# Optimization experiments

Measured on AMD Instinct MI355X. Metric: run time of the kernel, lower is better.

## Reference

```python
import jax, jax.numpy as jnp
import numpy as np

B, L = 8, 1024
VOCAB, D_ENC, D_MAIN = 260, 128, 256
N_ENC, N_MAIN, N_DEC, N_HEADS = 3, 6, 3, 4
N_RATIO = 6.0  # 1/target_ratio
NEG = jnp.float32(-1e9)


def setup_inputs() -> dict:
    key = jax.random.key(0)
    kc = iter(jax.random.split(key, 40))
    def nrm(shape, std):
        return jax.random.normal(next(kc), shape, jnp.float32) * std
    inp = {'byte_ids': jax.random.randint(next(kc), (B, L), 0, VOCAB)}
    inp['embed'] = nrm((VOCAB, D_ENC), D_ENC ** -0.5)
    eye = jnp.eye(D_ENC, dtype=jnp.float32)
    inp['wq'] = eye + nrm((D_ENC, D_ENC), 0.02)  # init is identity in the torch module
    inp['wk'] = eye + nrm((D_ENC, D_ENC), 0.02)
    inp['proj_up'] = nrm((D_MAIN, D_ENC), D_ENC ** -0.5)
    inp['proj_down'] = nrm((D_ENC, D_MAIN), 1e-3)
    inp['norm_w'] = jnp.ones((D_ENC,), jnp.float32)
    inp['norm_b'] = jnp.zeros((D_ENC,), jnp.float32)
    for pre, n, d in [('enc', N_ENC, D_ENC), ('main', N_MAIN, D_MAIN), ('dec', N_DEC, D_ENC)]:
        inp[pre + '_ln1_w'] = jnp.ones((n, d), jnp.float32)
        inp[pre + '_ln1_b'] = jnp.zeros((n, d), jnp.float32)
        inp[pre + '_qkv'] = nrm((n, 3 * d, d), d ** -0.5)   # MHA in_proj (3D, D)
        inp[pre + '_wo'] = nrm((n, d, d), d ** -0.5)        # MHA out_proj
        inp[pre + '_ln2_w'] = jnp.ones((n, d), jnp.float32)
        inp[pre + '_ln2_b'] = jnp.zeros((n, d), jnp.float32)
        inp[pre + '_w1'] = nrm((n, 2 * d, d), d ** -0.5)    # mlp_mult = 2
        inp[pre + '_w2'] = nrm((n, d, 2 * d), (2 * d) ** -0.5)
    return inp


def _ln(x, w, b):
    mu = jnp.mean(x, axis=-1, keepdims=True)
    var = jnp.mean((x - mu) ** 2, axis=-1, keepdims=True)
    return (x - mu) * jax.lax.rsqrt(var + 1e-5) * w + b


def _mha(x, wqkv, wo, bias):
    Bb, S, D = x.shape
    dh = D // N_HEADS
    q, k, v = jnp.split(x @ wqkv.T, 3, axis=-1)
    q = q.reshape(Bb, S, N_HEADS, dh)
    k = k.reshape(Bb, S, N_HEADS, dh)
    v = v.reshape(Bb, S, N_HEADS, dh)
    scores = jnp.einsum('bqhd,bkhd->bhqk', q, k) * (dh ** -0.5) + bias
    attn = jax.nn.softmax(scores, axis=-1)
    out = jnp.einsum('bhqk,bkhd->bqhd', attn, v).reshape(Bb, S, D)
    return out @ wo.T


def _block(x, stack, i, bias):
    ln1w, ln1b, qkv, wo, ln2w, ln2b, w1, w2 = (a[i] for a in stack)
    x = x + _mha(_ln(x, ln1w, ln1b), qkv, wo, bias)
    h = _ln(x, ln2w, ln2b)
    return x + jax.nn.gelu(h @ w1.T, approximate=False) @ w2.T


def _downsample(x, b_hard):
    # scatter boundary tokens to the front of a padded (B, S, D) buffer
    Bb, S, D = x.shape
    idx = jnp.cumsum(b_hard, axis=1).astype(jnp.int32) - 1
    dest = jnp.where(b_hard > 0.5, idx, S)  # S is out-of-range -> dropped
    def sc(xb, db):
        return jnp.zeros((S, D), xb.dtype).at[db].set(xb, mode='drop')
    out = jax.vmap(sc)(x, dest)
    counts = jnp.sum(b_hard, axis=1).astype(jnp.int32)
    mask = jnp.arange(S)[None, :] < counts[:, None]
    return out, mask


def _forward(byte_ids, embed, wq, wk,
             enc_ln1_w, enc_ln1_b, enc_qkv, enc_wo, enc_ln2_w, enc_ln2_b, enc_w1, enc_w2,
             proj_up,
             main_ln1_w, main_ln1_b, main_qkv, main_wo, main_ln2_w, main_ln2_b, main_w1, main_w2,
             proj_down,
             dec_ln1_w, dec_ln1_b, dec_qkv, dec_wo, dec_ln2_w, dec_ln2_b, dec_w1, dec_w2,
             norm_w, norm_b):
    causal = jnp.where(jnp.triu(jnp.ones((L, L), bool), 1), NEG, jnp.float32(0.0))[None, None]
    x = embed[byte_ids]  # (B, L, D_ENC)
    enc_p = (enc_ln1_w, enc_ln1_b, enc_qkv, enc_wo, enc_ln2_w, enc_ln2_b, enc_w1, enc_w2)
    for i in range(N_ENC):
        x = _block(x, enc_p, i, causal)

    # --- dynamic chunking (routing + ratio loss) ---
    def l2n(t):
        return t / jnp.maximum(jnp.linalg.norm(t, axis=-1, keepdims=True), 1e-12)
    q = l2n(x @ wq.T)
    k = l2n(x @ wk.T)
    k_prev = jnp.pad(k[:, :-1], ((0, 0), (1, 0), (0, 0)))
    cos = jnp.sum(q * k_prev, axis=-1)
    p = jnp.clip(0.5 * (1.0 - cos), 0.0, 1.0)
    p = jnp.concatenate([jnp.ones_like(p[:, :1]), p[:, 1:]], axis=1)
    b_hard = (p >= 0.5).astype(jnp.float32)
    N = N_RATIO
    F_act = jnp.mean(b_hard)
    G_act = jnp.mean(p)
    ratio_loss = N / (N - 1.0) * ((N - 1.0) * F_act * G_act + (1.0 - F_act) * (1.0 - G_act))
    compressed, comp_mask = _downsample(x, b_hard)
    p_comp = _downsample(p[..., None], b_hard)[0][..., 0]

    # --- main stack on compressed sequence (padded to L, masked) ---
    z = compressed @ proj_up.T
    main_bias = causal + jnp.where(comp_mask, jnp.float32(0.0), NEG)[:, None, None, :]
    main_p = (main_ln1_w, main_ln1_b, main_qkv, main_wo, main_ln2_w, main_ln2_b, main_w1, main_w2)
    for i in range(N_MAIN):
        z = _block(z, main_p, i, main_bias)
    z = z @ proj_down.T  # (B, L, D_ENC)

    # --- chunk-level EMA (parallel linear-recurrence scan) + gather + STE ---
    p_c = jnp.clip(p_comp, 1e-4, 1.0 - 1e-4)
    a = (1.0 - p_c).at[:, 0].set(0.0)[..., None]          # z_bar[0] = z[0]
    bv = (p_c[..., None] * z).at[:, :1].set(z[:, :1])
    def comb(lhs, rhs):
        al, bl = lhs
        ar, br = rhs
        return (al * ar, ar * bl + br)
    z_bar = jax.lax.associative_scan(comb, (a, bv), axis=1)[1]
    chunk_idx = jnp.clip(jnp.cumsum(b_hard, axis=1).astype(jnp.int32) - 1, 0, None)
    z_up = jnp.take_along_axis(z_bar, jnp.broadcast_to(chunk_idx[:, :, None], z_bar.shape), axis=1)
    c = b_hard * p + (1.0 - b_hard) * (1.0 - p)
    c_ste = c + jax.lax.stop_gradient(1.0 - c)
    x = x + c_ste[..., None] * z_up

    dec_p = (dec_ln1_w, dec_ln1_b, dec_qkv, dec_wo, dec_ln2_w, dec_ln2_b, dec_w1, dec_w2)
    for i in range(N_DEC):
        x = _block(x, dec_p, i, causal)
    x = _ln(x, norm_w, norm_b)
    logits = x @ embed.T  # tied head
    return logits, ratio_loss


def reference(byte_ids, embed, wq, wk,
              enc_ln1_w, enc_ln1_b, enc_qkv, enc_wo, enc_ln2_w, enc_ln2_b, enc_w1, enc_w2,
              proj_up,
              main_ln1_w, main_ln1_b, main_qkv, main_wo, main_ln2_w, main_ln2_b, main_w1, main_w2,
              proj_down,
              dec_ln1_w, dec_ln1_b, dec_qkv, dec_wo, dec_ln2_w, dec_ln2_b, dec_w1, dec_w2,
              norm_w, norm_b):
    return _forward(byte_ids, embed, wq, wk,
                    enc_ln1_w, enc_ln1_b, enc_qkv, enc_wo, enc_ln2_w, enc_ln2_b, enc_w1, enc_w2,
                    proj_up,
                    main_ln1_w, main_ln1_b, main_qkv, main_wo, main_ln2_w, main_ln2_b, main_w1, main_w2,
                    proj_down,
                    dec_ln1_w, dec_ln1_b, dec_qkv, dec_wo, dec_ln2_w, dec_ln2_b, dec_w1, dec_w2,
                    norm_w, norm_b)
```

## Files before the change

kernel.cpp:

```cpp
#include <hip/hip_runtime.h>
#include <hip/hip_bf16.h>

#define B_ 8
#define L_ 1024
#define BL (B_*L_)
#define DENC 128
#define DMAIN 256
#define VOCAB 260
#define NHEADS 4

typedef __hip_bfloat16 bf16;
typedef _Float16 f16;
typedef f16 half8 __attribute__((ext_vector_type(8)));
typedef f16 half4 __attribute__((ext_vector_type(4)));
typedef f16 half2v __attribute__((ext_vector_type(2)));
typedef float f32x4 __attribute__((ext_vector_type(4)));

__global__ __launch_bounds__(64) void k_detect(const void* __restrict__ emb, int* __restrict__ flag){
    int lane = threadIdx.x;
    const unsigned short* u = (const unsigned short*)emb;
    int bad = 0;
    #pragma unroll
    for (int j = 0; j < 4; j++){
        unsigned short h = u[lane + 64*j];
        bf16 t = *(const bf16*)&h;
        float v = __bfloat162float(t);
        if (!(fabsf(v) < 1e4f)) bad++;
    }
    #pragma unroll
    for (int o = 32; o >= 1; o >>= 1) bad += __shfl_xor(bad, o);
    if (lane == 0) flag[0] = (bad == 0) ? 1 : 0;
}

struct CvtArgs {
    const void* src[31];
    unsigned offs[32];
};
__global__ void k_cvt_all(CvtArgs a, float* __restrict__ dst, f16* __restrict__ dst16,
                          int total, const int* __restrict__ flag, unsigned f32mask){
    int isbf = flag[0];
    for (int i = blockIdx.x*256 + threadIdx.x; i < total; i += gridDim.x*256){
        int lo = 0, hi = 30;
        while (lo < hi){ int mid = (lo+hi+1)>>1; if (a.offs[mid] <= (unsigned)i) lo = mid; else hi = mid-1; }
        int j = i - (int)a.offs[lo];
        float v = isbf ? __bfloat162float(((const bf16*)a.src[lo])[j])
                       : ((const float*)a.src[lo])[j];
        if ((f32mask >> lo) & 1u) dst[i] = v;
        dst16[i] = (f16)v;
    }
}

__global__ __launch_bounds__(256) void k_embed_ln(const int* __restrict__ ids, const float* __restrict__ emb,
        const float* __restrict__ lnw, const float* __restrict__ lnb,
        float* __restrict__ x, f16* __restrict__ y){
    int row = blockIdx.x*4 + (threadIdx.x >> 6);
    int lane = threadIdx.x & 63;
    int id = ids[row];
    float v0 = emb[(size_t)id*DENC + lane];
    float v1 = emb[(size_t)id*DENC + 64 + lane];
    x[(size_t)row*DENC + lane] = v0;
    x[(size_t)row*DENC + 64 + lane] = v1;
    float s = v0 + v1;
    #pragma unroll
    for (int o=32;o>=1;o>>=1) s += __shfl_xor(s,o);
    float mu = s / (float)DENC;
    float d0 = v0-mu, d1 = v1-mu;
    float s2 = d0*d0 + d1*d1;
    #pragma unroll
    for (int o=32;o>=1;o>>=1) s2 += __shfl_xor(s2,o);
    float inv = rsqrtf(s2/(float)DENC + 1e-5f);
    y[(size_t)row*DENC + lane]      = (f16)(d0*inv*lnw[lane] + lnb[lane]);
    y[(size_t)row*DENC + 64 + lane] = (f16)(d1*inv*lnw[64+lane] + lnb[64+lane]);
}

template<int D>
__global__ __launch_bounds__(256) void k_ln16(const float* __restrict__ x, const float* __restrict__ w,
                                              const float* __restrict__ b, f16* __restrict__ y){
    int row = blockIdx.x*4 + (threadIdx.x >> 6);
    int lane = threadIdx.x & 63;
    const float* xr = x + (size_t)row*D;
    float v[D/64];
    float s = 0.f;
    #pragma unroll
    for (int j=0;j<D/64;j++){ v[j] = xr[lane + j*64]; s += v[j]; }
    #pragma unroll
    for (int o=32;o>=1;o>>=1) s += __shfl_xor(s,o);
    float mu = s / (float)D;
    float s2 = 0.f;
    #pragma unroll
    for (int j=0;j<D/64;j++){ float dd = v[j]-mu; s2 += dd*dd; }
    #pragma unroll
    for (int o=32;o>=1;o>>=1) s2 += __shfl_xor(s2,o);
    float inv = rsqrtf(s2/(float)D + 1e-5f);
    f16* yr = y + (size_t)row*D;
    #pragma unroll
    for (int j=0;j<D/64;j++){
        int d = lane + j*64;
        yr[d] = (f16)((v[j]-mu)*inv*w[d] + b[d]);
    }
}

#define GBM 64
#define GBN 64
#define GBK 32
__global__ __launch_bounds__(256) void k_gemm2(const float* __restrict__ A, const float* __restrict__ Wq,
        const float* __restrict__ Wk, float* __restrict__ Cq, float* __restrict__ Ck, int K)
{
    __shared__ float As[GBK][GBM+4];
    __shared__ float Ws[GBK][GBN+4];
    int tid = threadIdx.x;
    int bm = blockIdx.y * GBM;
    int bn = blockIdx.x * GBN;
    int tx = tid & 15, ty = tid >> 4;
    float acc[4][4] = {};
    for (int k0 = 0; k0 < K; k0 += GBK){
        #pragma unroll
        for (int i = tid; i < GBM*GBK; i += 256){
            int m = i >> 5, kk = i & 31;
            As[kk][m] = A[(size_t)(bm+m)*K + k0 + kk];
        }
        #pragma unroll
        for (int i = tid; i < GBN*GBK; i += 256){
            int n = i >> 5, kk = i & 31;
            int gn = bn + n;
            const float* W = (gn < 128) ? Wq : Wk;
            int wr = gn & 127;
            Ws[kk][n] = W[(size_t)wr*K + k0 + kk];
        }
        __syncthreads();
        #pragma unroll
        for (int kk = 0; kk < GBK; kk++){
            float a0[4], w0[4];
            *(float4*)a0 = *(const float4*)&As[kk][ty*4];
            *(float4*)w0 = *(const float4*)&Ws[kk][tx*4];
            #pragma unroll
            for (int i=0;i<4;i++)
                #pragma unroll
                for (int j=0;j<4;j++) acc[i][j] += a0[i]*w0[j];
        }
        __syncthreads();
    }
    #pragma unroll
    for (int i=0;i<4;i++){
        int m = bm + ty*4 + i;
        #pragma unroll
        for (int j=0;j<4;j++){
            int n = bn + tx*4 + j;
            float* C = (n < 128) ? Cq : Ck;
            C[(size_t)m*128 + (n & 127)] = acc[i][j];
        }
    }
}

template<int K>
__global__ __launch_bounds__(256) void k_hgemm(const f16* __restrict__ A, const f16* __restrict__ W,
        const float* __restrict__ R, float* __restrict__ C, f16* __restrict__ C16,
        void* __restrict__ OutRaw, const int* __restrict__ flag, int N, int mode,
        f16* __restrict__ Qd, f16* __restrict__ Kd, f16* __restrict__ Vd,
        int dShift, int dhShift)
{
    __shared__ half8 As[4][64];
    __shared__ half8 Ws[4][64];
    int tid = threadIdx.x;
    int wave = tid >> 6, lane = tid & 63;
    int wr = wave >> 1, wc = wave & 1;
    int quad = lane >> 4, l15 = lane & 15;
    int bm = blockIdx.y * 64, bn = blockIdx.x * 64;

    f32x4 acc[2][2] = {};
    int srow = tid >> 2, sc8 = tid & 3;
    const f16* ap0 = A + (size_t)(bm + srow)*K + sc8*8;
    int gn = bn + srow;
    const f16* wp0 = W + (size_t)gn*K + sc8*8;
    bool wok = (gn < N);

    for (int k0 = 0; k0 < K; k0 += 32){
        __syncthreads();
        As[sc8][srow] = *(const half8*)(ap0 + k0);
        Ws[sc8][srow] = wok ? *(const half8*)(wp0 + k0) : (half8)(f16)0.f;
        __syncthreads();
        half8 af[2], wf[2];
        af[0] = As[quad][wr*32 + l15];
        af[1] = As[quad][wr*32 + 16 + l15];
        wf[0] = Ws[quad][wc*32 + l15];
        wf[1] = Ws[quad][wc*32 + 16 + l15];
        #pragma unroll
        for (int i=0;i<2;i++)
            #pragma unroll
            for (int j=0;j<2;j++)
                acc[i][j] = __builtin_amdgcn_mfma_f32_16x16x32_f16(af[i], wf[j], acc[i][j], 0, 0, 0);
    }

    #pragma unroll
    for (int j=0;j<2;j++){
        int n = bn + wc*32 + j*16 + l15;
        if (n >= N) continue;
        #pragma unroll
        for (int i=0;i<2;i++){
            #pragma unroll
            for (int r=0;r<4;r++){
                int m = bm + wr*32 + i*16 + quad*4 + r;
                float v = acc[i][j][r];
                if (mode == 5){
                    int which = n >> dShift;
                    int rem = n & ((1<<dShift)-1);
                    int hh = rem >> dhShift;
                    int dd = rem & ((1<<dhShift)-1);
                    int bb = m >> 10, tt = m & 1023;
                    int Hn = 1 << (dShift - dhShift);
                    f16* dst = (which==0) ? Qd : ((which==1) ? Kd : Vd);
                    if (which == 2)
                        dst[((((size_t)bb*Hn + hh) << dhShift) + dd)*L_ + tt] = (f16)v;
                    else
                        dst[((((size_t)bb*Hn + hh)*L_ + tt) << dhShift) + dd] = (f16)v;
                    continue;
                }
                size_t off = (size_t)m*N + n;
                if (mode == 1){ C[off] = v + R[off]; }
                else if (mode == 2){
                    v = 0.5f*v*(1.0f + erff(v*0.70710678118654752f));
                    C16[off] = (f16)v;
                } else if (mode == 3){
                    if (flag[0]) ((bf16*)OutRaw)[off] = __float2bfloat16(v);
                    else         ((float*)OutRaw)[off] = v;
                } else C[off] = v;
            }
        }
    }
}

template<int K, int N>
__global__ __launch_bounds__(256) void k_gfl(const f16* __restrict__ A, const f16* __restrict__ W,
        const float* __restrict__ R, float* __restrict__ X, f16* __restrict__ Y,
        const float* __restrict__ lnw, const float* __restrict__ lnb, int doLN, int hasR)
{
    constexpr int NT2 = N/32;
    __shared__ half8 As[4][32];
    __shared__ half8 Ws[4][N];
    __shared__ float sred[2][2][32];
    int tid = threadIdx.x;
    int wave = tid >> 6, lane = tid & 63;
    int wr = wave >> 1, wc = wave & 1;
    int quad = lane >> 4, l15 = lane & 15;
    int bm = blockIdx.x * 32;

    f32x4 acc[NT2] = {};
    int srow = (tid & 127) >> 2, sch = tid & 3;
    const f16* ap0 = A + (size_t)(bm + srow)*K + sch*8;
    int s4 = tid >> 2;

    for (int k0 = 0; k0 < K; k0 += 32){
        __syncthreads();
        if (tid < 128) As[sch][srow] = *(const half8*)(ap0 + k0);
        #pragma unroll
        for (int s = 0; s < N/64; s++){
            int rr = s4 + s*64;
            Ws[sch][rr] = *(const half8*)(W + (size_t)rr*K + sch*8 + k0);
        }
        __syncthreads();
        half8 af = As[quad][wr*16 + l15];
        #pragma unroll
        for (int j=0;j<NT2;j++){
            half8 wf = Ws[quad][(wc*NT2 + j)*16 + l15];
            acc[j] = __builtin_amdgcn_mfma_f32_16x16x32_f16(af, wf, acc[j], 0, 0, 0);
        }
    }

    float v[NT2][4];
    #pragma unroll
    for (int r=0;r<4;r++){
        int row = bm + wr*16 + quad*4 + r;
        #pragma unroll
        for (int j=0;j<NT2;j++){
            int col = (wc*NT2 + j)*16 + l15;
            float rv = hasR ? R[(size_t)row*N + col] : 0.f;
            v[j][r] = acc[j][r] + rv;
            X[(size_t)row*N + col] = v[j][r];
        }
    }
    if (doLN){
        int lrow0 = wr*16 + quad*4;
        float mu[4], inv[4];
        #pragma unroll
        for (int r=0;r<4;r++){
            float s = 0.f;
            #pragma unroll
            for (int j=0;j<NT2;j++) s += v[j][r];
            s += __shfl_xor(s, 1); s += __shfl_xor(s, 2);
            s += __shfl_xor(s, 4); s += __shfl_xor(s, 8);
            if (l15 == 0) sred[0][wc][lrow0 + r] = s;
        }
        __syncthreads();
        #pragma unroll
        for (int r=0;r<4;r++)
            mu[r] = (sred[0][0][lrow0 + r] + sred[0][1][lrow0 + r]) / (float)N;
        #pragma unroll
        for (int r=0;r<4;r++){
            float s2 = 0.f;
            #pragma unroll
            for (int j=0;j<NT2;j++){ float dd = v[j][r] - mu[r]; s2 += dd*dd; }
            s2 += __shfl_xor(s2, 1); s2 += __shfl_xor(s2, 2);
            s2 += __shfl_xor(s2, 4); s2 += __shfl_xor(s2, 8);
            if (l15 == 0) sred[1][wc][lrow0 + r] = s2;
        }
        __syncthreads();
        #pragma unroll
        for (int r=0;r<4;r++)
            inv[r] = rsqrtf((sred[1][0][lrow0 + r] + sred[1][1][lrow0 + r]) / (float)N + 1e-5f);
        float wv_[NT2], bv_[NT2];
        #pragma unroll
        for (int j=0;j<NT2;j++){
            int col = (wc*NT2 + j)*16 + l15;
            wv_[j] = lnw[col];
            bv_[j] = lnb[col];
        }
        #pragma unroll
        for (int r=0;r<4;r++){
            int row = bm + wr*16 + quad*4 + r;
            #pragma unroll
            for (int j=0;j<NT2;j++){
                int col = (wc*NT2 + j)*16 + l15;
                Y[(size_t)row*N + col] = (f16)((v[j][r] - mu[r])*inv[r]*wv_[j] + bv_[j]);
            }
        }
    }
}

template<int K>
__global__ __launch_bounds__(256) void k_lngemm(const float* __restrict__ A, const f16* __restrict__ W,
        const float* __restrict__ lnw, const float* __restrict__ lnb, int doLN,
        float* __restrict__ C, void* __restrict__ OutRaw,
        const int* __restrict__ flag, int N, int mode)
{
    constexpr int SA = K + 8;
    constexpr int RPT = K/64;
    __shared__ f16 sA[64*SA];
    int tid = threadIdx.x;
    int wave = tid >> 6, lane = tid & 63;
    int wr = wave >> 1, wc = wave & 1;
    int quad = lane >> 4, l15 = lane & 15;
    int bm = blockIdx.y * 64, bn = blockIdx.x * 64;

    float wv_[RPT], bv_[RPT];
    #pragma unroll
    for (int j=0;j<RPT;j++){
        int d = lane*RPT + j;
        wv_[j] = doLN ? lnw[d] : 1.f;
        bv_[j] = doLN ? lnb[d] : 0.f;
    }
    for (int rr=0; rr<16; rr++){
        int row = wave*16 + rr;
        const float* xr = A + (size_t)(bm+row)*K + lane*RPT;
        float v[RPT];
        if (RPT==2){ float2 t = *(const float2*)xr; v[0]=t.x; v[1]=t.y; }
        else       { float4 t = *(const float4*)xr; v[0]=t.x; v[1]=t.y; v[2]=t.z; v[3]=t.w; }
        float mu = 0.f, inv = 1.f;
        if (doLN){
            float s=0.f;
            #pragma unroll
            for (int j=0;j<RPT;j++) s += v[j];
            #pragma unroll
            for (int o=32;o>=1;o>>=1) s += __shfl_xor(s,o);
            mu = s / (float)K;
            float s2=0.f;
            #pragma unroll
            for (int j=0;j<RPT;j++){ float dd=v[j]-mu; s2+=dd*dd; }
            #pragma unroll
            for (int o=32;o>=1;o>>=1) s2 += __shfl_xor(s2,o);
            inv = rsqrtf(s2/(float)K + 1e-5f);
        }
        if (RPT==2){
            half2v h;
            h[0]=(f16)((v[0]-mu)*inv*wv_[0]+bv_[0]);
            h[1]=(f16)((v[1]-mu)*inv*wv_[1]+bv_[1]);
            *(half2v*)&sA[row*SA + lane*2] = h;
        } else {
            half4 h;
            #pragma unroll
            for (int j=0;j<4;j++) h[j]=(f16)((v[j]-mu)*inv*wv_[j]+bv_[j]);
            *(half4*)&sA[row*SA + lane*4] = h;
        }
    }
    __syncthreads();

    f32x4 acc[2][2] = {};
    int n0 = bn + wc*32 + l15;
    bool ok0 = n0 < N, ok1 = (n0+16) < N;
    const f16* w0p = W + (size_t)n0*K + quad*8;
    const f16* w1p = W + (size_t)(n0+16)*K + quad*8;
    #pragma unroll 4
    for (int k0=0;k0<K;k0+=32){
        half8 af[2], wf[2];
        af[0] = *(const half8*)&sA[(wr*32 + l15)*SA + k0 + quad*8];
        af[1] = *(const half8*)&sA[(wr*32 + 16 + l15)*SA + k0 + quad*8];
        wf[0] = ok0 ? *(const half8*)(w0p + k0) : (half8)(f16)0.f;
        wf[1] = ok1 ? *(const half8*)(w1p + k0) : (half8)(f16)0.f;
        #pragma unroll
        for (int i=0;i<2;i++)
            #pragma unroll
            for (int j=0;j<2;j++)
                acc[i][j] = __builtin_amdgcn_mfma_f32_16x16x32_f16(af[i], wf[j], acc[i][j], 0, 0, 0);
    }

    #pragma unroll
    for (int j=0;j<2;j++){
        int n = bn + wc*32 + j*16 + l15;
        if (n >= N) continue;
        #pragma unroll
        for (int i=0;i<2;i++){
            #pragma unroll
            for (int r=0;r<4;r++){
                int m = bm + wr*32 + i*16 + quad*4 + r;
                float v = acc[i][j][r];
                size_t off = (size_t)m*N + n;
                if (mode == 3){
                    if (flag[0]) ((bf16*)OutRaw)[off] = __float2bfloat16(v);
                    else         ((float*)OutRaw)[off] = v;
                } else C[off] = v;
            }
        }
    }
}

template<int DH>
__global__ __launch_bounds__(256) void k_mflash(const f16* __restrict__ Qh, const f16* __restrict__ Kh,
        const f16* __restrict__ Vt, f16* __restrict__ out, const int* __restrict__ counts,
        float scale)
{
    constexpr int BQ = 64, BK = 64;
    constexpr int RS = DH + 8;
    constexpr int PS = BK + 8;
    __shared__ f16 sQ[BQ*RS];
    __shared__ f16 sK[BK*RS];
    __shared__ f16 sVt[DH*PS];
    __shared__ f16 sP[BQ*PS];

    int x = blockIdx.x, b = x >> 2, h = x & 3;
    int yy = blockIdx.y;
    int qt = (yy < 8) ? yy : 23 - yy;
    int q0 = qt * BQ;
    int tid = threadIdx.x;
    int wv = tid >> 6, lane = tid & 63;
    int quad = lane >> 4, l15 = lane & 15;

    const f16* Qb = Qh + (size_t)x*L_*DH;
    const f16* Kb = Kh + (size_t)x*L_*DH;
    const f16* Vb = Vt + (size_t)x*DH*L_;
    int kcap = counts ? counts[b] : L_;
    int klen = min(kcap, q0 + BQ);

    for (int i = tid; i < BQ*DH/8; i += 256){
        int r = (8*i)/DH, c = (8*i)%DH;
        *(half8*)&sQ[r*RS + c] = *(const half8*)&Qb[(size_t)(q0+r)*DH + c];
    }

    float m[4], l[4];
    #pragma unroll
    for (int r=0;r<4;r++){ m[r] = -1e30f; l[r] = 0.f; }
    f32x4 accO[DH/16] = {};

    for (int k0 = 0; k0 < klen; k0 += BK){
        __syncthreads();
        for (int i = tid; i < BK*DH/8; i += 256){
            int r = (8*i)/DH, c = (8*i)%DH;
            *(half8*)&sK[r*RS + c] = *(const half8*)&Kb[(size_t)(k0+r)*DH + c];
        }
        for (int i = tid; i < DH*BK/8; i += 256){
            int r = (8*i)/BK, c = (8*i)%BK;
            *(half8*)&sVt[r*PS + c] = *(const half8*)&Vb[(size_t)r*L_ + k0 + c];
        }
        __syncthreads();

        half8 af[DH/32];
        #pragma unroll
        for (int ds=0; ds<DH/32; ds++)
            af[ds] = *(const half8*)&sQ[(16*wv + l15)*RS + quad*8 + 32*ds];
        f32x4 accS[4] = {};
        #pragma unroll
        for (int t=0;t<4;t++){
            #pragma unroll
            for (int ds=0; ds<DH/32; ds++){
                half8 bf = *(const half8*)&sK[(16*t + l15)*RS + quad*8 + 32*ds];
                accS[t] = __builtin_amdgcn_mfma_f32_16x16x32_f16(af[ds], bf, accS[t], 0, 0, 0);
            }
        }

        #pragma unroll
        for (int r=0;r<4;r++){
            int qrow = q0 + 16*wv + quad*4 + r;
            float sv[4];
            #pragma unroll
            for (int t=0;t<4;t++){
                float v = accS[t][r]*scale;
                int kp = k0 + 16*t + l15;
                if (kp > qrow || kp >= kcap) v = -1e30f;
                sv[t] = v;
            }
            float rm = fmaxf(fmaxf(sv[0],sv[1]), fmaxf(sv[2],sv[3]));
            rm = fmaxf(rm, __shfl_xor(rm, 1));
            rm = fmaxf(rm, __shfl_xor(rm, 2));
            rm = fmaxf(rm, __shfl_xor(rm, 4));
            rm = fmaxf(rm, __shfl_xor(rm, 8));
            float mn = fmaxf(m[r], rm);
            float al = __expf(m[r] - mn);
            float p0 = __expf(sv[0]-mn), p1 = __expf(sv[1]-mn);
            float p2 = __expf(sv[2]-mn), p3 = __expf(sv[3]-mn);
            float rs = p0+p1+p2+p3;
            rs += __shfl_xor(rs, 1);
            rs += __shfl_xor(rs, 2);
            rs += __shfl_xor(rs, 4);
            rs += __shfl_xor(rs, 8);
            l[r] = l[r]*al + rs;
            m[r] = mn;
            #pragma unroll
            for (int dt=0; dt<DH/16; dt++) accO[dt][r] *= al;
            int prow = 16*wv + quad*4 + r;
            sP[prow*PS + 16*0 + l15] = (f16)p0;
            sP[prow*PS + 16*1 + l15] = (f16)p1;
            sP[prow*PS + 16*2 + l15] = (f16)p2;
            sP[prow*PS + 16*3 + l15] = (f16)p3;
        }

        half8 pf[2];
        #pragma unroll
        for (int ks=0; ks<2; ks++)
            pf[ks] = *(const half8*)&sP[(16*wv + l15)*PS + quad*8 + 32*ks];
        #pragma unroll
        for (int dt=0; dt<DH/16; dt++){
            #pragma unroll
            for (int ks=0; ks<2; ks++){
                half8 bv = *(const half8*)&sVt[(16*dt + l15)*PS + quad*8 + 32*ks];
                accO[dt] = __builtin_amdgcn_mfma_f32_16x16x32_f16(pf[ks], bv, accO[dt], 0, 0, 0);
            }
        }
    }

    #pragma unroll
    for (int r=0;r<4;r++){
        float inv = 1.0f / l[r];
        int qrow = q0 + 16*wv + quad*4 + r;
        #pragma unroll
        for (int dt=0; dt<DH/16; dt++){
            int d = 16*dt + l15;
            out[((size_t)b*L_ + qrow)*(NHEADS*DH) + h*DH + d] = (f16)(accO[dt][r]*inv);
        }
    }
}

__global__ __launch_bounds__(64) void k_router(const float* __restrict__ Q, const float* __restrict__ Kr,
        float* __restrict__ p, float* __restrict__ bh, float* __restrict__ acc)
{
    int idx = blockIdx.x;
    int t = idx & (L_-1);
    int lane = threadIdx.x;
    if (idx == 0 && lane < 8) acc[lane] = 0.f;
    float pv;
    if (t == 0){ pv = 1.0f; }
    else {
        const float* qr = Q  + (size_t)idx*DENC;
        const float* kr = Kr + (size_t)(idx-1)*DENC;
        float qq=0.f, kk=0.f, qk=0.f;
        #pragma unroll
        for (int j=0;j<2;j++){
            float qv = qr[lane + j*64], kv = kr[lane + j*64];
            qq += qv*qv; kk += kv*kv; qk += qv*kv;
        }
        #pragma unroll
        for (int o=32;o>=1;o>>=1){ qq += __shfl_xor(qq,o); kk += __shfl_xor(kk,o); qk += __shfl_xor(qk,o); }
        float cosv = qk / (fmaxf(sqrtf(qq),1e-12f)*fmaxf(sqrtf(kk),1e-12f));
        pv = 0.5f*(1.0f - cosv);
        pv = fminf(fmaxf(pv, 0.0f), 1.0f);
    }
    if (lane == 0){ p[idx] = pv; bh[idx] = (pv >= 0.5f) ? 1.0f : 0.0f; }
}

__global__ __launch_bounds__(64) void k_seq(const float* __restrict__ bh, const float* __restrict__ p,
                      int* __restrict__ cidx, int* __restrict__ src, int* __restrict__ counts,
                      float* __restrict__ acc){
    int b = blockIdx.x;
    int lane = threadIdx.x;
    int base = b*L_ + lane*16;
    int h[16];
    int cnt = 0;
    float ps = 0.f;
    #pragma unroll
    for (int j=0;j<16;j++){ h[j] = bh[base+j] > 0.5f; cnt += h[j]; ps += p[base+j]; }
    int inc = cnt;
    #pragma unroll
    for (int o=1;o<64;o<<=1){ int nb = __shfl_up(inc, o); if (lane >= o) inc += nb; }
    int run = inc - cnt;
    #pragma unroll
    for (int j=0;j<16;j++){
        run += h[j];
        int ci = run - 1; if (ci < 0) ci = 0;
        cidx[base+j] = ci;
        if (h[j]) src[b*L_ + run-1] = lane*16 + j;
    }
    float cs = (float)cnt;
    #pragma unroll
    for (int o=32;o>=1;o>>=1){ ps += __shfl_xor(ps,o); cs += __shfl_xor(cs,o); }
    if (lane == 0){ atomicAdd(&acc[0], ps); atomicAdd(&acc[1], cs); }
    if (lane == 63) counts[b] = inc;
}

__global__ __launch_bounds__(128) void k_scatter2(const float* __restrict__ x, const float* __restrict__ p,
        const int* __restrict__ src, const int* __restrict__ counts,
        f16* __restrict__ comp, float* __restrict__ pcomp)
{
    int s = blockIdx.x & (L_-1), b = blockIdx.x >> 10, d = threadIdx.x;
    int cnt = counts[b];
    f16* crow = comp + ((size_t)b*L_ + s)*DENC;
    if (s < cnt){
        int t = src[b*L_ + s];
        crow[d] = (f16)x[((size_t)b*L_ + t)*DENC + d];
        if (d == 0) pcomp[b*L_ + s] = p[b*L_ + t];
    } else {
        crow[d] = (f16)0.f;
        if (d == 0) pcomp[b*L_ + s] = 0.f;
    }
}

__global__ __launch_bounds__(256) void k_ema2(const float* __restrict__ z, const float* __restrict__ pcomp,
                                              float* __restrict__ zbar){
    __shared__ float sp[L_];
    int blk = blockIdx.x;
    int b = blk >> 5;
    int tid = threadIdx.x, wv = tid >> 6, lane = tid & 63;
    int d = ((blk & 31) << 2) + wv;
    for (int i = tid; i < L_; i += 256){
        float pc = pcomp[b*L_ + i];
        sp[i] = fminf(fmaxf(pc, 1e-4f), 1.0f - 1e-4f);
    }
    __syncthreads();
    const float* zb = z + ((size_t)b*L_)*DENC + d;
    int t0 = lane*16;
    float zv[16];
    #pragma unroll
    for (int i=0;i<16;i++) zv[i] = zb[(size_t)(t0+i)*DENC];
    float A = 1.f, Bv = 0.f;
    #pragma unroll
    for (int i=0;i<16;i++){
        int t = t0 + i;
        float pc = sp[t];
        float a  = (t==0) ? 0.f : (1.f - pc);
        float bb = (t==0) ? zv[i] : pc*zv[i];
        A = a*A;
        Bv = a*Bv + bb;
    }
    #pragma unroll
    for (int off=1; off<64; off<<=1){
        float Ap = __shfl_up(A, off);
        float Bp = __shfl_up(Bv, off);
        if (lane >= off){ Bv = A*Bp + Bv; A = A*Ap; }
    }
    float sin_ = __shfl_up(Bv, 1);
    if (lane == 0) sin_ = 0.f;
    float s = sin_;
    float* ob = zbar + ((size_t)b*L_)*DENC + d;
    #pragma unroll
    for (int i=0;i<16;i++){
        int t = t0 + i;
        float pc = sp[t];
        float a  = (t==0) ? 0.f : (1.f - pc);
        float bb = (t==0) ? zv[i] : pc*zv[i];
        s = a*s + bb;
        ob[(size_t)t*DENC] = s;
    }
}

__global__ __launch_bounds__(256) void k_combine_ln(float* __restrict__ x, const float* __restrict__ zbar,
        const int* __restrict__ cidx, const float* __restrict__ lnw, const float* __restrict__ lnb,
        f16* __restrict__ y){
    int row = blockIdx.x*4 + (threadIdx.x >> 6);
    int lane = threadIdx.x & 63;
    int b = row >> 10;
    int ci = cidx[row];
    const float* zr = zbar + ((size_t)b*L_ + ci)*DENC;
    float v0 = x[(size_t)row*DENC + lane]      + zr[lane];
    float v1 = x[(size_t)row*DENC + 64 + lane] + zr[64 + lane];
    x[(size_t)row*DENC + lane] = v0;
    x[(size_t)row*DENC + 64 + lane] = v1;
    float s = v0 + v1;
    #pragma unroll
    for (int o=32;o>=1;o>>=1) s += __shfl_xor(s,o);
    float mu = s / (float)DENC;
    float d0 = v0-mu, d1 = v1-mu;
    float s2 = d0*d0 + d1*d1;
    #pragma unroll
    for (int o=32;o>=1;o>>=1) s2 += __shfl_xor(s2,o);
    float inv = rsqrtf(s2/(float)DENC + 1e-5f);
    y[(size_t)row*DENC + lane]      = (f16)(d0*inv*lnw[lane] + lnb[lane]);
    y[(size_t)row*DENC + 64 + lane] = (f16)(d1*inv*lnw[64+lane] + lnb[64+lane]);
}

__global__ void k_loss(const float* __restrict__ acc, void* __restrict__ out, const int* __restrict__ flag){
    float G = acc[0] / (float)BL;
    float F = acc[1] / (float)BL;
    float ratio = 1.2f*(5.0f*F*G + (1.0f-F)*(1.0f-G));
    if (flag[0]) ((bf16*)out)[(size_t)BL*VOCAB] = __float2bfloat16(ratio);
    else         ((float*)out)[(size_t)BL*VOCAB] = ratio;
}

extern "C" void kernel_launch(void* const* d_in, const int* in_sizes, int n_in,
                              void* d_out, int out_size, void* d_ws, size_t ws_size,
                              hipStream_t stream) {
    (void)out_size; (void)ws_size;
    const int* byte_ids = (const int*)d_in[0];

    float* ws = (float*)d_ws;
    size_t off = 0;
    int* FLAG = (int*)ws; off += 16;
    float* W32 = ws + off;

    k_detect<<<1, 64, 0, stream>>>(d_in[1], FLAG);

    CvtArgs ca;
    const float* w32[32];
    unsigned woff = 0;
    for (int i = 1; i < n_in && i < 32; i++){
        w32[i] = W32 + woff;
        ca.src[i-1] = d_in[i];
        ca.offs[i-1] = woff;
        woff += (unsigned)in_sizes[i];
    }
    ca.offs[31] = woff;
    off += woff;
    f16* W16h = (f16*)(ws + off); off += (woff+1)/2;
    const f16* w16[32];
    for (int i = 1; i < n_in && i < 32; i++) w16[i] = W16h + ca.offs[i-1];
    k_cvt_all<<<2048, 256, 0, stream>>>(ca, W32, W16h, (int)woff, FLAG, 0x199999E7u);

    const float* embed    = w32[1];
    const float* wq       = w32[2];
    const float* wk       = w32[3];
    const float* norm_w   = w32[6];
    const float* norm_b   = w32[7];

    float* X    = ws + off; off += (size_t)BL*DENC;
    float* QKVf = ws + off; off += (size_t)BL*3*DMAIN;
    float* ATTf = ws + off; off += (size_t)BL*DMAIN;
    float* Hf   = ws + off; off += (size_t)BL*2*DMAIN;
    float* LNf  = ws + off; off += (size_t)BL*DMAIN;
    float* Z    = ws + off; off += (size_t)BL*DMAIN;
    float* COMPf= ws + off; off += (size_t)BL*DENC;
    float* P    = ws + off; off += BL;
    float* BH   = ws + off; off += BL;
    float* PCOMP= ws + off; off += BL;
    float* ACC  = ws + off; off += 8;
    int* CIDX   = (int*)(ws + off); off += BL;
    int* SRC    = (int*)(ws + off); off += BL;
    int* COUNTS = (int*)(ws + off); off += 64;

    f16* QKV16 = (f16*)QKVf;
    f16* ATT16 = (f16*)ATTf;
    f16* H16   = (f16*)Hf;
    f16* LN16  = (f16*)LNf;
    f16* COMP16= (f16*)COMPf;
    float* Qr  = ATTf;
    float* Kr  = Hf;
    float* ZDN = QKVf;
    float* ZBAR= QKVf + (size_t)BL*DENC;

    auto hgemm = [&](int K, const f16* A, const f16* W, const float* R, float* C, f16* C16,
                     void* Ob, int N, int mode, f16* Qd, f16* Kd, f16* Vd, int dS, int dhS){
        dim3 g((N+63)/64, BL/64);
        if (K == 128)      k_hgemm<128><<<g,256,0,stream>>>(A, W, R, C, C16, Ob, FLAG, N, mode, Qd, Kd, Vd, dS, dhS);
        else if (K == 256) k_hgemm<256><<<g,256,0,stream>>>(A, W, R, C, C16, Ob, FLAG, N, mode, Qd, Kd, Vd, dS, dhS);
        else               k_hgemm<512><<<g,256,0,stream>>>(A, W, R, C, C16, Ob, FLAG, N, mode, Qd, Kd, Vd, dS, dhS);
    };
    auto gfl = [&](int K, int N, const f16* A, const f16* W, const float* R, float* Xo, f16* Y,
                   const float* lw, const float* lb, int doLN, int hasR){
        dim3 g(BL/32);
        if (K == 128 && N == 128)      k_gfl<128,128><<<g,256,0,stream>>>(A, W, R, Xo, Y, lw, lb, doLN, hasR);
        else if (K == 256 && N == 128) k_gfl<256,128><<<g,256,0,stream>>>(A, W, R, Xo, Y, lw, lb, doLN, hasR);
        else if (K == 128 && N == 256) k_gfl<128,256><<<g,256,0,stream>>>(A, W, R, Xo, Y, lw, lb, doLN, hasR);
        else if (K == 256 && N == 256) k_gfl<256,256><<<g,256,0,stream>>>(A, W, R, Xo, Y, lw, lb, doLN, hasR);
        else                           k_gfl<512,256><<<g,256,0,stream>>>(A, W, R, Xo, Y, lw, lb, doLN, hasR);
    };

    auto block128 = [&](float* Xs, const f16* qkvw, const f16* wo,
                        const float* l2w, const float* l2b, const f16* w1, const f16* w2,
                        const float* nlw, const float* nlb, int doNext){
        hgemm(128, LN16, qkvw, nullptr, nullptr, nullptr, nullptr, 3*DENC, 5,
              QKV16, QKV16 + (size_t)BL*DENC, QKV16 + (size_t)2*BL*DENC, 7, 5);
        k_mflash<32><<<dim3(B_*NHEADS,16),256,0,stream>>>(QKV16, QKV16 + (size_t)BL*DENC,
                                                          QKV16 + (size_t)2*BL*DENC,
                                                          ATT16, nullptr, 0.17677669529663687f);
        gfl(128, 128, ATT16, wo, Xs, Xs, LN16, l2w, l2b, 1, 1);
        hgemm(128, LN16, w1, nullptr, nullptr, H16, nullptr, 2*DENC, 2, nullptr, nullptr, nullptr, 0, 0);
        gfl(256, 128, H16, w2, Xs, Xs, LN16, nlw, nlb, doNext, 1);
    };
    auto block_main = [&](float* Xs, const f16* qkvw, const f16* wo,
                          const float* l2w, const float* l2b, const f16* w1, const f16* w2,
                          const float* nlw, const float* nlb, int doNext){
        hgemm(256, LN16, qkvw, nullptr, nullptr, nullptr, nullptr, 3*DMAIN, 5,
              QKV16, QKV16 + (size_t)BL*DMAIN, QKV16 + (size_t)2*BL*DMAIN, 8, 6);
        k_mflash<64><<<dim3(B_*NHEADS,16),256,0,stream>>>(QKV16, QKV16 + (size_t)BL*DMAIN,
                                                          QKV16 + (size_t)2*BL*DMAIN,
                                                          ATT16, COUNTS, 0.125f);
        gfl(256, 256, ATT16, wo, Xs, Xs, LN16, l2w, l2b, 1, 1);
        hgemm(256, LN16, w1, nullptr, nullptr, H16, nullptr, 2*DMAIN, 2, nullptr, nullptr, nullptr, 0, 0);
        gfl(512, 256, H16, w2, Xs, Xs, LN16, nlw, nlb, doNext, 1);
    };

    k_embed_ln<<<BL/4, 256, 0, stream>>>(byte_ids, embed, w32[8], w32[9], X, LN16);
    for (int i = 0; i < 3; i++)
        block128(X, w16[10] + (size_t)i*3*DENC*DENC, w16[11] + (size_t)i*DENC*DENC,
                 w32[12] + i*DENC, w32[13] + i*DENC,
                 w16[14] + (size_t)i*2*DENC*DENC, w16[15] + (size_t)i*2*DENC*DENC,
                 (i < 2) ? w32[8] + (i+1)*DENC : nullptr,
                 (i < 2) ? w32[9] + (i+1)*DENC : nullptr, (i < 2) ? 1 : 0);

    k_gemm2<<<dim3(4, BL/64), 256, 0, stream>>>(X, wq, wk, Qr, Kr, DENC);
    k_router<<<BL, 64, 0, stream>>>(Qr, Kr, P, BH, ACC);
    k_seq<<<B_, 64, 0, stream>>>(BH, P, CIDX, SRC, COUNTS, ACC);
    k_scatter2<<<BL, 128, 0, stream>>>(X, P, SRC, COUNTS, COMP16, PCOMP);

    gfl(128, 256, COMP16, w16[4], nullptr, Z, LN16, w32[16], w32[17], 1, 0);
    for (int i = 0; i < 6; i++)
        block_main(Z, w16[18] + (size_t)i*3*DMAIN*DMAIN, w16[19] + (size_t)i*DMAIN*DMAIN,
                   w32[20] + i*DMAIN, w32[21] + i*DMAIN,
                   w16[22] + (size_t)i*2*DMAIN*DMAIN, w16[23] + (size_t)i*2*DMAIN*DMAIN,
                   (i < 5) ? w32[16] + (i+1)*DMAIN : nullptr,
                   (i < 5) ? w32[17] + (i+1)*DMAIN : nullptr, (i < 5) ? 1 : 0);
    k_lngemm<256><<<dim3(2, BL/64), 256, 0, stream>>>(Z, w16[5], nullptr, nullptr, 0,
                                                      ZDN, nullptr, FLAG, DENC, 0);

    k_ema2<<<256, 256, 0, stream>>>(ZDN, PCOMP, ZBAR);
    k_combine_ln<<<BL/4, 256, 0, stream>>>(X, ZBAR, CIDX, w32[24], w32[25], LN16);

    for (int i = 0; i < 3; i++)
        block128(X, w16[26] + (size_t)i*3*DENC*DENC, w16[27] + (size_t)i*DENC*DENC,
                 w32[28] + i*DENC, w32[29] + i*DENC,
                 w16[30] + (size_t)i*2*DENC*DENC, w16[31] + (size_t)i*2*DENC*DENC,
                 (i < 2) ? w32[24] + (i+1)*DENC : norm_w,
                 (i < 2) ? w32[25] + (i+1)*DENC : norm_b, 1);

    hgemm(128, LN16, w16[1], nullptr, nullptr, nullptr, d_out, VOCAB, 3,
          nullptr, nullptr, nullptr, 0, 0);
    k_loss<<<1,1,0,stream>>>(ACC, d_out, FLAG);
}
```

Measured before the change: 1.168 ms.

## Fuse MLP up-projection, GELU and down-projection into one kernel

Replaces the separate up-projection GEMM (GELU epilogue writing the hidden tensor to global memory) and the down-projection GEMM with residual and LayerNorm epilogue with a single k_mlp kernel per 32-row tile. The GELU hidden activations stay in shared memory instead of making a round trip through global memory, and one launch per block is removed. Unused kernels and GEMM epilogue modes are also deleted. In exchange, each workgroup reloads both weight matrices, the staging loads have no pipelining and take many barriers, and the large shared-memory footprint may lower occupancy.

Result: no change. 1.187 ms (+1.6%).

```diff
diff --git a/kernel.cpp b/kernel.cpp
--- a/kernel.cpp
+++ b/kernel.cpp
@@ -71,33 +71,6 @@
     float inv = rsqrtf(s2/(float)DENC + 1e-5f);
     y[(size_t)row*DENC + lane]      = (f16)(d0*inv*lnw[lane] + lnb[lane]);
     y[(size_t)row*DENC + 64 + lane] = (f16)(d1*inv*lnw[64+lane] + lnb[64+lane]);
-}
-
-template<int D>
-__global__ __launch_bounds__(256) void k_ln16(const float* __restrict__ x, const float* __restrict__ w,
-                                              const float* __restrict__ b, f16* __restrict__ y){
-    int row = blockIdx.x*4 + (threadIdx.x >> 6);
-    int lane = threadIdx.x & 63;
-    const float* xr = x + (size_t)row*D;
-    float v[D/64];
-    float s = 0.f;
-    #pragma unroll
-    for (int j=0;j<D/64;j++){ v[j] = xr[lane + j*64]; s += v[j]; }
-    #pragma unroll
-    for (int o=32;o>=1;o>>=1) s += __shfl_xor(s,o);
-    float mu = s / (float)D;
-    float s2 = 0.f;
-    #pragma unroll
-    for (int j=0;j<D/64;j++){ float dd = v[j]-mu; s2 += dd*dd; }
-    #pragma unroll
-    for (int o=32;o>=1;o>>=1) s2 += __shfl_xor(s2,o);
-    float inv = rsqrtf(s2/(float)D + 1e-5f);
-    f16* yr = y + (size_t)row*D;
-    #pragma unroll
-    for (int j=0;j<D/64;j++){
-        int d = lane + j*64;
-        yr[d] = (f16)((v[j]-mu)*inv*w[d] + b[d]);
-    }
 }
 
 #define GBM 64
@@ -216,11 +189,7 @@
                     continue;
                 }
                 size_t off = (size_t)m*N + n;
-                if (mode == 1){ C[off] = v + R[off]; }
-                else if (mode == 2){
-                    v = 0.5f*v*(1.0f + erff(v*0.70710678118654752f));
-                    C16[off] = (f16)v;
-                } else if (mode == 3){
+                if (mode == 3){
                     if (flag[0]) ((bf16*)OutRaw)[off] = __float2bfloat16(v);
                     else         ((float*)OutRaw)[off] = v;
                 } else C[off] = v;
@@ -321,6 +290,136 @@
             for (int j=0;j<NT2;j++){
                 int col = (wc*NT2 + j)*16 + l15;
                 Y[(size_t)row*N + col] = (f16)((v[j][r] - mu[r])*inv[r]*wv_[j] + bv_[j]);
+            }
+        }
+    }
+}
+
+template<int K, int NH>
+__global__ __launch_bounds__(256) void k_mlp(const f16* __restrict__ A, const f16* __restrict__ W1,
+        const f16* __restrict__ W2, const float* __restrict__ R, float* __restrict__ X,
+        f16* __restrict__ Y, const float* __restrict__ lnw, const float* __restrict__ lnb, int doLN)
+{
+    constexpr int NO = K;
+    constexpr int SA = K + 16;
+    constexpr int SH = NH + 16;
+    constexpr int WR = (NO > 128) ? NO : 128;
+    constexpr int NT2 = NO/32;
+    __shared__ f16 sA[32*SA];
+    __shared__ f16 sH[32*SH];
+    __shared__ half8 Ws[4][WR];
+    __shared__ float sred[2][2][32];
+
+    int tid = threadIdx.x;
+    int wave = tid >> 6, lane = tid & 63;
+    int wr = wave >> 1, wc = wave & 1;
+    int quad = lane >> 4, l15 = lane & 15;
+    int bm = blockIdx.x * 32;
+
+    for (int s = tid; s < 32*(K/8); s += 256){
+        int row = s / (K/8), c8 = s % (K/8);
+        *(half8*)&sA[row*SA + c8*8] = *(const half8*)&A[(size_t)(bm+row)*K + c8*8];
+    }
+
+    for (int cg = 0; cg < NH/128; cg++){
+        f32x4 acc1[4] = {};
+        for (int k0 = 0; k0 < K; k0 += 32){
+            __syncthreads();
+            for (int s = tid; s < 512; s += 256){
+                int row = s >> 2, sch = s & 3;
+                Ws[sch][row] = *(const half8*)&W1[(size_t)(cg*128+row)*K + k0 + sch*8];
+            }
+            __syncthreads();
+            half8 af = *(const half8*)&sA[(wr*16 + l15)*SA + k0 + quad*8];
+            #pragma unroll
+            for (int j=0;j<4;j++){
+                half8 wf = Ws[quad][(wc*4 + j)*16 + l15];
+                acc1[j] = __builtin_amdgcn_mfma_f32_16x16x32_f16(af, wf, acc1[j], 0, 0, 0);
+            }
+        }
+        #pragma unroll
+        for (int j=0;j<4;j++){
+            #pragma unroll
+            for (int r=0;r<4;r++){
+                float v = acc1[j][r];
+                v = 0.5f*v*(1.0f + erff(v*0.70710678118654752f));
+                int row = wr*16 + quad*4 + r;
+                int col = cg*128 + (wc*4 + j)*16 + l15;
+                sH[row*SH + col] = (f16)v;
+            }
+        }
+    }
+
+    f32x4 acc2[NT2] = {};
+    for (int k2 = 0; k2 < NH; k2 += 32){
+        __syncthreads();
+        for (int s = tid; s < 4*NO; s += 256){
+            int row = s >> 2, sch = s & 3;
+            Ws[sch][row] = *(const half8*)&W2[(size_t)row*NH + k2 + sch*8];
+        }
+        __syncthreads();
+        half8 af = *(const half8*)&sH[(wr*16 + l15)*SH + k2 + quad*8];
+        #pragma unroll
+        for (int j=0;j<NT2;j++){
+            half8 wf = Ws[quad][(wc*NT2 + j)*16 + l15];
+            acc2[j] = __builtin_amdgcn_mfma_f32_16x16x32_f16(af, wf, acc2[j], 0, 0, 0);
+        }
+    }
+
+    float v[NT2][4];
+    #pragma unroll
+    for (int r=0;r<4;r++){
+        int row = bm + wr*16 + quad*4 + r;
+        #pragma unroll
+        for (int j=0;j<NT2;j++){
+            int col = (wc*NT2 + j)*16 + l15;
+            v[j][r] = acc2[j][r] + R[(size_t)row*NO + col];
+            X[(size_t)row*NO + col] = v[j][r];
+        }
+    }
+    if (doLN){
+        int lrow0 = wr*16 + quad*4;
+        float mu[4], inv[4];
+        #pragma unroll
+        for (int r=0;r<4;r++){
+            float s = 0.f;
+            #pragma unroll
+            for (int j=0;j<NT2;j++) s += v[j][r];
+            s += __shfl_xor(s, 1); s += __shfl_xor(s, 2);
+            s += __shfl_xor(s, 4); s += __shfl_xor(s, 8);
+            if (l15 == 0) sred[0][wc][lrow0 + r] = s;
+        }
+        __syncthreads();
+        #pragma unroll
+        for (int r=0;r<4;r++)
+            mu[r] = (sred[0][0][lrow0 + r] + sred[0][1][lrow0 + r]) / (float)NO;
+        #pragma unroll
+        for (int r=0;r<4;r++){
+            float s2 = 0.f;
+            #pragma unroll
+            for (int j=0;j<NT2;j++){ float dd = v[j][r] - mu[r]; s2 += dd*dd; }
+            s2 += __shfl_xor(s2, 1); s2 += __shfl_xor(s2, 2);
+            s2 += __shfl_xor(s2, 4); s2 += __shfl_xor(s2, 8);
+            if (l15 == 0) sred[1][wc][lrow0 + r] = s2;
+        }
+        __syncthreads();
+        #pragma unroll
+        for (int r=0;r<4;r++)
+            inv[r] = rsqrtf((sred[1][0][lrow0 + r] + sred[1][1][lrow0 + r]) / (float)NO + 1e-5f);
+        float wv_[NT2], bv_[NT2];
+        #pragma unroll
+        for (int j=0;j<NT2;j++){
+            int col = (wc*NT2 + j)*16 + l15;
+            wv_[j] = lnw[col];
+            bv_[j] = lnb[col];
+        }
+        #pragma unroll
+        for (int r=0;r<4;r++){
+            int row = bm + wr*16 + quad*4 + r;
+            #pragma unroll
+            for (int j=0;j<NT2;j++){
+                int col = (wc*NT2 + j)*16 + l15;
+                Y[(size_t)row*NO + col] = (f16)((v[j][r] - mu[r])*inv[r]*wv_[j] + bv_[j]);
             }
         }
     }
@@ -753,7 +852,6 @@
 
     f16* QKV16 = (f16*)QKVf;
     f16* ATT16 = (f16*)ATTf;
-    f16* H16   = (f16*)Hf;
     f16* LN16  = (f16*)LNf;
     f16* COMP16= (f16*)COMPf;
     float* Qr  = ATTf;
@@ -772,10 +870,9 @@
                    const float* lw, const float* lb, int doLN, int hasR){
         dim3 g(BL/32);
         if (K == 128 && N == 128)      k_gfl<128,128><<<g,256,0,stream>>>(A, W, R, Xo, Y, lw, lb, doLN, hasR);
-        else if (K == 256 && N == 128) k_gfl<256,128><<<g,256,0,stream>>>(A, W, R, Xo, Y, lw, lb, doLN, hasR);
+        else if (K == 256 && N == 256) k_gfl<256,256><<<g,256,0,stream>>>(A, W, R, Xo, Y, lw, lb, doLN, hasR);
         else if (K == 128 && N == 256) k_gfl<128,256><<<g,256,0,stream>>>(A, W, R, Xo, Y, lw, lb, doLN, hasR);
-        else if (K == 256 && N == 256) k_gfl<256,256><<<g,256,0,stream>>>(A, W, R, Xo, Y, lw, lb, doLN, hasR);
-        else                           k_gfl<512,256><<<g,256,0,stream>>>(A, W, R, Xo, Y, lw, lb, doLN, hasR);
+        else                           k_gfl<256,128><<<g,256,0,stream>>>(A, W, R, Xo, Y, lw, lb, doLN, hasR);
     };
 
     auto block128 = [&](float* Xs, const f16* qkvw, const f16* wo,
@@ -787,8 +884,7 @@
                                                           QKV16 + (size_t)2*BL*DENC,
                                                           ATT16, nullptr, 0.17677669529663687f);
         gfl(128, 128, ATT16, wo, Xs, Xs, LN16, l2w, l2b, 1, 1);
-        hgemm(128, LN16, w1, nullptr, nullptr, H16, nullptr, 2*DENC, 2, nullptr, nullptr, nullptr, 0, 0);
-        gfl(256, 128, H16, w2, Xs, Xs, LN16, nlw, nlb, doNext, 1);
+        k_mlp<128,256><<<BL/32,256,0,stream>>>(LN16, w1, w2, Xs, Xs, LN16, nlw, nlb, doNext);
     };
     auto block_main = [&](float* Xs, const f16* qkvw, const f16* wo,
                           const float* l2w, const float* l2b, const f16* w1, const f16* w2,
@@ -799,8 +895,7 @@
                                                           QKV16 + (size_t)2*BL*DMAIN,
                                                           ATT16, COUNTS, 0.125f);
         gfl(256, 256, ATT16, wo, Xs, Xs, LN16, l2w, l2b, 1, 1);
-        hgemm(256, LN16, w1, nullptr, nullptr, H16, nullptr, 2*DMAIN, 2, nullptr, nullptr, nullptr, 0, 0);
-        gfl(512, 256, H16, w2, Xs, Xs, LN16, nlw, nlb, doNext, 1);
+        k_mlp<256,512><<<BL/32,256,0,stream>>>(LN16, w1, w2, Xs, Xs, LN16, nlw, nlb, doNext);
     };
 
     k_embed_ln<<<BL/4, 256, 0, stream>>>(byte_ids, embed, w32[8], w32[9], X, LN16);
```
